# Kernel tuning notes

Measured on AMD Instinct MI355X. Metric: run time of the kernel, lower is better.

## Reference

```python
import jax, jax.numpy as jnp
import numpy as np

TOPK = 5

def setup_inputs() -> dict:
    key = jax.random.key(0)
    k1, k2, k3 = jax.random.split(key, 3)
    x = jax.random.normal(k1, (32, 256, 28, 28), jnp.float32)
    gamma = jnp.ones((256,), jnp.float32)
    beta = jnp.zeros((256,), jnp.float32)
    conv_w = jax.random.normal(k2, (256, 256), jnp.float32) * 0.02
    conv_b = jax.random.normal(k3, (256,), jnp.float32) * 0.02
    return {"x": x, "gamma": gamma, "beta": beta, "conv_w": conv_w, "conv_b": conv_b, "snip": 8}


def reference(x, gamma, beta, conv_w, conv_b, snip):
    BS, C, H, W = x.shape
    B = BS // snip
    THW = snip * H * W
    identity = x
    # [B_S,C,H,W] -> [B,C,THW] grouping snip frames per clip
    xs = x.reshape(B, snip, C, H, W).transpose(0, 2, 1, 3, 4).reshape(B, C, THW)
    # cosine correlation: x^T x / (|x_t| |x_s|)
    up = jnp.einsum('bct,bcs->bts', xs, xs)                    # [B,THW,THW]
    nrm = jnp.sqrt(jnp.sum(xs * xs, axis=1))                   # [B,THW]
    corr = up / (nrm[:, :, None] * nrm[:, None, :])
    # mask per-frame diagonal blocks with -1 (exclude same-frame matches)
    blk = jnp.arange(THW) // (H * W)
    diag_block = blk[:, None] == blk[None, :]                  # [THW,THW]
    corr = jnp.where(diag_block[None], jnp.float32(-1.0), corr)
    # torch.topk(corr, k, dim=1): top-k along rows for each column j.
    # corr is symmetric post-mask; implement via top_k on transposed last axis.
    _, idx = jax.lax.top_k(corr.transpose(0, 2, 1), TOPK)      # [B,THW,k]
    idx = idx.transpose(0, 2, 1)                               # [B,k,THW]
    # gather: out[b,i,c,j] = xs[b,c, idx[b,i,j]]  (slicecollect, vectorized)
    gathered = jnp.take_along_axis(xs[:, None], idx[:, :, None, :], axis=3)  # [B,k,C,THW]
    y = gathered.max(axis=1)                                   # [B,C,THW] ('max' mode)
    y = y.reshape(B, C, snip, H, W).transpose(0, 2, 1, 3, 4).reshape(BS, C, H, W)
    # BatchNorm2d (training-mode batch stats, eps=1e-5)
    mean = y.mean(axis=(0, 2, 3))
    var = y.var(axis=(0, 2, 3))
    y = (y - mean[None, :, None, None]) * jax.lax.rsqrt(var + 1e-5)[None, :, None, None]
    y = y * gamma[None, :, None, None] + beta[None, :, None, None]
    y = jax.nn.relu(y)
    # 1x1 conv
    y = jnp.einsum('bchw,oc->bohw', y, conv_w) + conv_b[None, :, None, None]
    return y + identity
```

## Files before the change

kernel.cpp:

```cpp
#include <hip/hip_runtime.h>
#include <cfloat>
#include <cmath>

#define B_    4
#define SNIP  8
#define CCH   256
#define HW    784
#define THW   6272
#define NROWS 25088
#define TOPK  5
#define NTILE 49
#define NPAIR 1225

typedef _Float16 f16;
typedef f16   half8 __attribute__((ext_vector_type(8)));
typedef f16   half4 __attribute__((ext_vector_type(4)));
typedef float f32x4 __attribute__((ext_vector_type(4)));

__device__ __forceinline__ void ins5(float key, int idx, float tv[TOPK], int ti[TOPK]) {
    const bool c4 = key > tv[4];
    const bool c3 = key > tv[3];
    const bool c2 = key > tv[2];
    const bool c1 = key > tv[1];
    const bool c0 = key > tv[0];
    tv[4] = c3 ? tv[3] : (c4 ? key : tv[4]);
    ti[4] = c3 ? ti[3] : (c4 ? idx : ti[4]);
    tv[3] = c2 ? tv[2] : (c3 ? key : tv[3]);
    ti[3] = c2 ? ti[2] : (c3 ? idx : ti[3]);
    tv[2] = c1 ? tv[1] : (c2 ? key : tv[2]);
    ti[2] = c1 ? ti[1] : (c2 ? idx : ti[2]);
    tv[1] = c0 ? tv[0] : (c1 ? key : tv[1]);
    ti[1] = c0 ? ti[0] : (c1 ? idx : ti[1]);
    tv[0] = c0 ? key  : tv[0];
    ti[0] = c0 ? idx  : ti[0];
}

__device__ __forceinline__ void async16(const void* g, void* l) {
    __builtin_amdgcn_global_load_lds(
        (const __attribute__((address_space(1))) void*)g,
        (__attribute__((address_space(3))) void*)l, 16, 0, 0);
}

__global__ __launch_bounds__(256)
void transpose_norm_split_kernel(const float* __restrict__ x, f16* __restrict__ Xs,
                                 float* __restrict__ nrm) {
    __shared__ float T[256][33];
    const int bs = blockIdx.x;
    const int p0 = blockIdx.y * 32;
    const int b = bs >> 3, f = bs & 7;
    const int tid = threadIdx.x;

    const int pl = tid & 31, ch = tid >> 5;
    const int p = p0 + pl;
    if (p < HW) {
#pragma unroll
        for (int cc = 0; cc < 32; ++cc) {
            const int c = cc * 8 + ch;
            T[c][pl] = x[((size_t)bs * CCH + c) * HW + p];
        }
    }
    __syncthreads();

    const int rloc = tid >> 3, k = tid & 7;
    const int gp = p0 + rloc;
    const size_t trow = (size_t)b * THW + (size_t)f * HW + gp;

    float s = 0.0f;
    if (gp < HW) {
#pragma unroll
        for (int j = 0; j < 32; ++j) {
            const float v = T[k * 32 + j][rloc];
            s += v * v;
        }
    }
    s += __shfl_xor(s, 1, 64);
    s += __shfl_xor(s, 2, 64);
    s += __shfl_xor(s, 4, 64);

    if (gp < HW) {
        const float sq = sqrtf(s);
        const float rs = 1.0f / sq;
        if (k == 0) nrm[trow] = sq;
#pragma unroll
        for (int q = 0; q < 4; ++q) {
            half8 hv, lv;
#pragma unroll
            for (int j = 0; j < 8; ++j) {
                const float v = T[k * 32 + q * 8 + j][rloc] * rs;
                const f16 h = (f16)v;
                hv[j] = h;
                lv[j] = (f16)(v - (float)h);
            }
            *(half8*)(Xs + trow * 512 + k * 32 + q * 8) = hv;
            *(half8*)(Xs + trow * 512 + 256 + k * 32 + q * 8) = lv;
        }
    }
}

__device__ __forceinline__ void block_merge_store(
    const float (*tv)[TOPK], const int (*ti)[TOPK], char* smem,
    int tid, int wid, int q, int wc, int lm,
    int rslot, size_t gcol0,
    float* __restrict__ pval, unsigned short* __restrict__ pidx) {
    float* Mv = (float*)smem;
    unsigned short* Mi = (unsigned short*)(smem + 21120);
    const int slot = (wid >> 1) * 4 + q;
    __syncthreads();
#pragma unroll
    for (int j = 0; j < 4; ++j) {
        const int c128 = wc + 16 * j + lm;
#pragma unroll
        for (int s = 0; s < TOPK; ++s) {
            Mv[(slot * TOPK + s) * 132 + c128] = tv[j][s];
            Mi[(slot * TOPK + s) * 132 + c128] = (unsigned short)ti[j][s];
        }
    }
    __syncthreads();
    if (tid < 128) {
        float bv5[TOPK]; int bi5[TOPK];
#pragma unroll
        for (int s = 0; s < TOPK; ++s) { bv5[s] = -FLT_MAX; bi5[s] = 0; }
        for (int s = 0; s < 40; ++s) ins5(Mv[s * 132 + tid], (int)Mi[s * 132 + tid], bv5, bi5);
#pragma unroll
        for (int s = 0; s < TOPK; ++s) {
            const size_t o = ((size_t)(rslot * TOPK + s)) * NROWS + gcol0 + tid;
            pval[o] = bv5[s];
            pidx[o] = (unsigned short)bi5[s];
        }
    }
}

__global__ __launch_bounds__(256, 3)
void gram_sym_kernel(const f16* __restrict__ Xs,
                     float* __restrict__ pval, unsigned short* __restrict__ pidx) {
    __shared__ __align__(16) char smem[33280];
    f16* As = (f16*)smem;
    f16* Bs = As + 8192;
    float* TT = (float*)smem;

    const int tid = threadIdx.x;
    const int lane = tid & 63, wid = tid >> 6;
    const int wr = (wid >> 1) * 64, wc = (wid & 1) * 64;
    const int lm = lane & 15, q = lane >> 4;
    const int lm7 = lm & 7;
    const int b = blockIdx.z;

    const int p = blockIdx.x;
    int cj = (int)((sqrtf(8.0f * (float)p + 1.0f) - 1.0f) * 0.5f);
    while ((cj + 1) * (cj + 2) / 2 <= p) ++cj;
    while (cj * (cj + 1) / 2 > p) --cj;
    const int ri = p - cj * (cj + 1) / 2;
    const int t0 = ri * 128, j0 = cj * 128;

    const size_t bbase = (size_t)b * THW;
    const f16* Xb = Xs + bbase * 512;

    const int srow = tid >> 3;
    const int skk = (((tid & 7) ^ (srow & 7)) * 8);

    int loj[4];
#pragma unroll
    for (int j = 0; j < 4; ++j) loj[j] = ((j0 + wc + 16 * j + lm) / HW) * HW;

    float tv[4][TOPK];
    int   ti[4][TOPK];
#pragma unroll
    for (int j = 0; j < 4; ++j)
#pragma unroll
        for (int s = 0; s < TOPK; ++s) { tv[j][s] = -FLT_MAX; ti[j][s] = 0; }

    const int segA[3] = {0, 256, 0};
    const int segB[3] = {0, 0, 256};

    f32x4 acc[4][4];
#pragma unroll
    for (int i = 0; i < 4; ++i)
#pragma unroll
        for (int j = 0; j < 4; ++j) acc[i][j] = (f32x4)0.0f;

    for (int cc = 0; cc < 12; ++cc) {
        const int seg = cc >> 2, k64 = (cc & 3) * 64;
        const int aoff = segA[seg] + k64 + skk;
        const int boff = segB[seg] + k64 + skk;
#pragma unroll
        for (int pp = 0; pp < 4; ++pp)
            async16(Xb + (size_t)(t0 + srow + 32 * pp) * 512 + aoff,
                    smem + wid * 1024 + pp * 4096);
#pragma unroll
        for (int pp = 0; pp < 4; ++pp)
            async16(Xb + (size_t)(j0 + srow + 32 * pp) * 512 + boff,
                    smem + 16384 + wid * 1024 + pp * 4096);
        __syncthreads();
#pragma unroll
        for (int ks = 0; ks < 2; ++ks) {
            const int ku = (((4 * ks + q) ^ lm7) * 8);
            half8 av[4], bv[4];
#pragma unroll
            for (int i = 0; i < 4; ++i)
                av[i] = *(const half8*)(As + (wr + 16 * i + lm) * 64 + ku);
#pragma unroll
            for (int j = 0; j < 4; ++j)
                bv[j] = *(const half8*)(Bs + (wc + 16 * j + lm) * 64 + ku);
#pragma unroll
            for (int i = 0; i < 4; ++i)
#pragma unroll
                for (int j = 0; j < 4; ++j)
                    acc[i][j] = __builtin_amdgcn_mfma_f32_16x16x32_f16(av[i], bv[j], acc[i][j], 0, 0, 0);
        }
        __syncthreads();
    }

#pragma unroll
    for (int i = 0; i < 4; ++i) {
        const int tb = t0 + wr + 16 * i + 4 * q;
#pragma unroll
        for (int reg = 0; reg < 4; ++reg) {
            const int t = tb + reg;
#pragma unroll
            for (int j = 0; j < 4; ++j) {
                const float key = ((unsigned)(t - loj[j]) < (unsigned)HW)
                                  ? -FLT_MAX : acc[i][j][reg];
                ins5(key, t, tv[j], ti[j]);
            }
        }
    }
    block_merge_store(tv, ti, smem, tid, wid, q, wc, lm,
                      ri, bbase + (size_t)j0, pval, pidx);

    if (ri != cj) {
        int lo2[4];
#pragma unroll
        for (int j = 0; j < 4; ++j) lo2[j] = ((t0 + wc + 16 * j + lm) / HW) * HW;
        float tv2[4][TOPK];
        int   ti2[4][TOPK];
#pragma unroll
        for (int j = 0; j < 4; ++j)
#pragma unroll
            for (int s = 0; s < TOPK; ++s) { tv2[j][s] = -FLT_MAX; ti2[j][s] = 0; }
        const int wrb = wid >> 1;
#pragma unroll
        for (int h = 0; h < 2; ++h) {
            __syncthreads();
            if ((wid & 1) == h) {
#pragma unroll
                for (int i = 0; i < 4; ++i)
#pragma unroll
                    for (int j = 0; j < 4; ++j)
#pragma unroll
                        for (int reg = 0; reg < 4; ++reg)
                            TT[(wr + 16 * i + 4 * q + reg) * 65 + 16 * j + lm] = acc[i][j][reg];
            }
            __syncthreads();
#pragma unroll
            for (int ii = 0; ii < 2; ++ii) {
                const int spb = wrb * 32 + 16 * ii + 4 * q;
                const int sg0 = j0 + 64 * h + spb;
#pragma unroll
                for (int reg = 0; reg < 4; ++reg) {
                    const int sg = sg0 + reg;
#pragma unroll
                    for (int j = 0; j < 4; ++j) {
                        const float raw = TT[(wc + 16 * j + lm) * 65 + spb + reg];
                        const float key = ((unsigned)(sg - lo2[j]) < (unsigned)HW)
                                          ? -FLT_MAX : raw;
                        ins5(key, sg, tv2[j], ti2[j]);
                    }
                }
            }
        }
        block_merge_store(tv2, ti2, smem, tid, wid, q, wc, lm,
                          cj, bbase + (size_t)t0, pval, pidx);
    }
}

__global__ __launch_bounds__(256)
void merge_topk_sym_kernel(const float* __restrict__ pval, const unsigned short* __restrict__ pidx,
                           int* __restrict__ idx5) {
    __shared__ float Lv[4][TOPK][64];
    __shared__ unsigned short Li[4][TOPK][64];
    const int tid = threadIdx.x;
    const int part = tid >> 6, cl = tid & 63;
    const int col = blockIdx.x * 64 + cl;

    float bv5[TOPK]; int bi5[TOPK];
#pragma unroll
    for (int s = 0; s < TOPK; ++s) { bv5[s] = -FLT_MAX; bi5[s] = 0; }

    const int r0 = part * 13;
    const int r1 = (r0 + 13 < NTILE) ? r0 + 13 : NTILE;
    for (int r = r0; r < r1; ++r) {
#pragma unroll
        for (int s = 0; s < TOPK; ++s) {
            const size_t o = ((size_t)(r * TOPK + s)) * NROWS + col;
            ins5(pval[o], (int)pidx[o], bv5, bi5);
        }
    }
#pragma unroll
    for (int s = 0; s < TOPK; ++s) { Lv[part][s][cl] = bv5[s]; Li[part][s][cl] = (unsigned short)bi5[s]; }
    __syncthreads();
    if (tid < 64) {
        float cv[TOPK]; int ci[TOPK];
#pragma unroll
        for (int s = 0; s < TOPK; ++s) { cv[s] = -FLT_MAX; ci[s] = 0; }
#pragma unroll
        for (int pp = 0; pp < 4; ++pp)
#pragma unroll
            for (int s = 0; s < TOPK; ++s) ins5(Lv[pp][s][tid], (int)Li[pp][s][tid], cv, ci);
        int* op = idx5 + (size_t)col * TOPK;
#pragma unroll
        for (int s = 0; s < TOPK; ++s) op[s] = ci[s];
    }
}

__global__ __launch_bounds__(256)
void gather_bn_kernel(const f16* __restrict__ Xs, const float* __restrict__ nrm,
                      const int* __restrict__ idx5,
                      f16* __restrict__ yf, float* __restrict__ partial) {
    __shared__ float ls[2][4][256];
    const int tid = threadIdx.x;
    const int wid = tid >> 6, lane = tid & 63;
    const int row0 = blockIdx.x * 32 + wid * 8;
    float s1x = 0, s1y = 0, s1z = 0, s1w = 0;
    float s2x = 0, s2y = 0, s2z = 0, s2w = 0;
    for (int rr = 0; rr < 8; ++rr) {
        const int row = row0 + rr;
        const int b = row / THW;
        const int* id = idx5 + (size_t)row * TOPK;
        const f16* base = Xs + (size_t)b * THW * 512;
        const float* nb = nrm + (size_t)b * THW;
        float4 m = make_float4(-FLT_MAX, -FLT_MAX, -FLT_MAX, -FLT_MAX);
#pragma unroll
        for (int i = 0; i < TOPK; ++i) {
            const int t = id[i];
            const float nv = nb[t];
            const f16* rp = base + (size_t)t * 512 + lane * 4;
            const half4 h = *(const half4*)rp;
            const half4 l = *(const half4*)(rp + 256);
            m.x = fmaxf(m.x, ((float)h.x + (float)l.x) * nv);
            m.y = fmaxf(m.y, ((float)h.y + (float)l.y) * nv);
            m.z = fmaxf(m.z, ((float)h.z + (float)l.z) * nv);
            m.w = fmaxf(m.w, ((float)h.w + (float)l.w) * nv);
        }
        half4 ym; ym.x = (f16)m.x; ym.y = (f16)m.y; ym.z = (f16)m.z; ym.w = (f16)m.w;
        *(half4*)(yf + (size_t)row * CCH + lane * 4) = ym;
        s1x += m.x; s1y += m.y; s1z += m.z; s1w += m.w;
        s2x += m.x * m.x; s2y += m.y * m.y; s2z += m.z * m.z; s2w += m.w * m.w;
    }
    *(float4*)&ls[0][wid][lane * 4] = make_float4(s1x, s1y, s1z, s1w);
    *(float4*)&ls[1][wid][lane * 4] = make_float4(s2x, s2y, s2z, s2w);
    __syncthreads();
    const float a  = ls[0][0][tid] + ls[0][1][tid] + ls[0][2][tid] + ls[0][3][tid];
    const float b2 = ls[1][0][tid] + ls[1][1][tid] + ls[1][2][tid] + ls[1][3][tid];
    partial[(size_t)blockIdx.x * 512 + tid] = a;
    partial[(size_t)blockIdx.x * 512 + 256 + tid] = b2;
}

__global__ __launch_bounds__(256)
void bn_final_kernel(const float* __restrict__ partial, const float* __restrict__ gamma,
                     const float* __restrict__ beta, float* __restrict__ ab) {
    const int c = blockIdx.x;
    const int tid = threadIdx.x;
    float s1 = 0, s2 = 0;
    for (int p = tid; p < 784; p += 256) {
        s1 += partial[(size_t)p * 512 + c];
        s2 += partial[(size_t)p * 512 + 256 + c];
    }
    __shared__ float r1[256], r2[256];
    r1[tid] = s1; r2[tid] = s2;
    __syncthreads();
    for (int off = 128; off > 0; off >>= 1) {
        if (tid < off) { r1[tid] += r1[tid + off]; r2[tid] += r2[tid + off]; }
        __syncthreads();
    }
    if (tid == 0) {
        const float inv_n = 1.0f / 25088.0f;
        const float mean = r1[0] * inv_n;
        const float var  = r2[0] * inv_n - mean * mean;
        const float a = gamma[c] / sqrtf(var + 1e-5f);
        ab[c] = a;
        ab[256 + c] = beta[c] - mean * a;
    }
}

__global__ __launch_bounds__(256, 2)
void conv_f16_kernel(const f16* __restrict__ yf, const float* __restrict__ w,
                     const float* __restrict__ ab, const float* __restrict__ cb,
                     const float* __restrict__ x, float* __restrict__ out) {
    __shared__ __align__(16) f16 smem[2 * 128 * 64];
    f16* As = smem;
    f16* Ws = smem + 8192;

    const int tid = threadIdx.x;
    const int lane = tid & 63, wid = tid >> 6;
    const int wr = (wid >> 1) * 64, wc = (wid & 1) * 64;
    const int lm = lane & 15, q = lane >> 4;
    const int lm7 = lm & 7;
    const int R0 = blockIdx.x * 128;
    const int o0 = blockIdx.y * 128;
    const int g8 = (tid & 7) * 8;
    const int sr = tid >> 3;

    f32x4 acc[4][4];
#pragma unroll
    for (int i = 0; i < 4; ++i)
#pragma unroll
        for (int j = 0; j < 4; ++j) acc[i][j] = (f32x4)0.0f;

    float cbv[4];
#pragma unroll
    for (int j = 0; j < 4; ++j) cbv[j] = cb[o0 + wc + 16 * j + lm];

    for (int kc = 0; kc < CCH; kc += 64) {
        const int cbase = kc + g8;
        const float4 sa0 = *(const float4*)(ab + cbase);
        const float4 sa1 = *(const float4*)(ab + cbase + 4);
        const float4 sb0 = *(const float4*)(ab + 256 + cbase);
        const float4 sb1 = *(const float4*)(ab + 256 + cbase + 4);
#pragma unroll
        for (int p = 0; p < 4; ++p) {
            const int r = sr + 32 * p;
            const half8 hv = *(const half8*)(yf + (size_t)(R0 + r) * CCH + cbase);
            half8 z;
            z[0] = (f16)fmaxf(fmaf((float)hv[0], sa0.x, sb0.x), 0.0f);
            z[1] = (f16)fmaxf(fmaf((float)hv[1], sa0.y, sb0.y), 0.0f);
            z[2] = (f16)fmaxf(fmaf((float)hv[2], sa0.z, sb0.z), 0.0f);
            z[3] = (f16)fmaxf(fmaf((float)hv[3], sa0.w, sb0.w), 0.0f);
            z[4] = (f16)fmaxf(fmaf((float)hv[4], sa1.x, sb1.x), 0.0f);
            z[5] = (f16)fmaxf(fmaf((float)hv[5], sa1.y, sb1.y), 0.0f);
            z[6] = (f16)fmaxf(fmaf((float)hv[6], sa1.z, sb1.z), 0.0f);
            z[7] = (f16)fmaxf(fmaf((float)hv[7], sa1.w, sb1.w), 0.0f);
            *(half8*)(As + r * 64 + (((tid & 7) ^ (r & 7)) * 8)) = z;
        }
#pragma unroll
        for (int p = 0; p < 4; ++p) {
            const int ol = sr + 32 * p;
            const float4 w0 = *(const float4*)(w + (size_t)(o0 + ol) * CCH + cbase);
            const float4 w1 = *(const float4*)(w + (size_t)(o0 + ol) * CCH + cbase + 4);
            half8 z;
            z[0] = (f16)w0.x; z[1] = (f16)w0.y; z[2] = (f16)w0.z; z[3] = (f16)w0.w;
            z[4] = (f16)w1.x; z[5] = (f16)w1.y; z[6] = (f16)w1.z; z[7] = (f16)w1.w;
            *(half8*)(Ws + ol * 64 + (((tid & 7) ^ (ol & 7)) * 8)) = z;
        }
        __syncthreads();
#pragma unroll
        for (int ks = 0; ks < 2; ++ks) {
            const int ku = (((4 * ks + q) ^ lm7) * 8);
            half8 av[4], bv[4];
#pragma unroll
            for (int i = 0; i < 4; ++i)
                av[i] = *(const half8*)(As + (wr + 16 * i + lm) * 64 + ku);
#pragma unroll
            for (int j = 0; j < 4; ++j)
                bv[j] = *(const half8*)(Ws + (wc + 16 * j + lm) * 64 + ku);
#pragma unroll
            for (int i = 0; i < 4; ++i)
#pragma unroll
                for (int j = 0; j < 4; ++j)
                    acc[i][j] = __builtin_amdgcn_mfma_f32_16x16x32_f16(av[i], bv[j], acc[i][j], 0, 0, 0);
        }
        __syncthreads();
    }
#pragma unroll
    for (int i = 0; i < 4; ++i) {
#pragma unroll
        for (int reg = 0; reg < 4; ++reg) {
            const int R = R0 + wr + 16 * i + 4 * q + reg;
            const int bs = R / HW;
            const int hw = R - bs * HW;
#pragma unroll
            for (int j = 0; j < 4; ++j) {
                const int o = o0 + wc + 16 * j + lm;
                const size_t oi = ((size_t)bs * CCH + o) * HW + hw;
                out[oi] = acc[i][j][reg] + cbv[j] + x[oi];
            }
        }
    }
}

extern "C" void kernel_launch(void* const* d_in, const int* in_sizes, int n_in,
                              void* d_out, int out_size, void* d_ws, size_t ws_size,
                              hipStream_t stream) {
    const float* x      = (const float*)d_in[0];
    const float* gamma  = (const float*)d_in[1];
    const float* beta   = (const float*)d_in[2];
    const float* conv_w = (const float*)d_in[3];
    const float* conv_b = (const float*)d_in[4];
    float* out = (float*)d_out;

    float* ws = (float*)d_ws;
    f16*   Xsp  = (f16*)ws;
    f16*   yf   = (f16*)(ws + 6422528);
    float* nrm  = ws + 9633792;
    float* part = ws + 9658880;
    float* ab   = ws + 10060288;
    int*   idx5 = (int*)(ws + 10060800);
    float* pvalS = ws + 10186240;
    unsigned short* pidxS = (unsigned short*)(ws + 16332800);

    transpose_norm_split_kernel<<<dim3(32, 25), 256, 0, stream>>>(x, Xsp, nrm);
    gram_sym_kernel<<<dim3(NPAIR, 1, B_), 256, 0, stream>>>(Xsp, pvalS, pidxS);
    merge_topk_sym_kernel<<<NROWS / 64, 256, 0, stream>>>(pvalS, pidxS, idx5);
    gather_bn_kernel<<<NROWS / 32, 256, 0, stream>>>(Xsp, nrm, idx5, yf, part);
    bn_final_kernel<<<256, 256, 0, stream>>>(part, gamma, beta, ab);
    conv_f16_kernel<<<dim3(NROWS / 128, 2), 256, 0, stream>>>(yf, conv_w, ab, conv_b, x, out);
}
```

Baseline: 418.8 us.

## Skip diagonal-block masking on off-diagonal tiles and swizzle transpose scratch for occupancy

Computes per tile whether its row and column frame ranges overlap, and uses a template-specialised epilogue that drops the per-element same-frame mask test when they do not. The padded 65-stride transpose scratch becomes a 64-stride rotated-column swizzle, so shared memory fits in 32 KB. Launch bounds go from 3 to 4 blocks per SM. The higher occupancy target may force register spills given the large accumulator and top-k state, and having two epilogue copies increases code size.

```diff
diff --git a/kernel.cpp b/kernel.cpp
--- a/kernel.cpp
+++ b/kernel.cpp
@@ -41,6 +41,49 @@
         (__attribute__((address_space(3))) void*)l, 16, 0, 0);
 }
 
+__device__ __forceinline__ int tta(int row, int col) {
+    return (row << 6) | ((col + row) & 63);
+}
+
+template<bool FM>
+__device__ __forceinline__ void epi_norm(const f32x4 (&acc)[4][4], int t0wrq, const int (&loj)[4],
+                                         float (&tv)[4][TOPK], int (&ti)[4][TOPK]) {
+#pragma unroll
+    for (int i = 0; i < 4; ++i) {
+#pragma unroll
+        for (int reg = 0; reg < 4; ++reg) {
+            const int t = t0wrq + 16 * i + reg;
+#pragma unroll
+            for (int j = 0; j < 4; ++j) {
+                float key = acc[i][j][reg];
+                if (FM) key = ((unsigned)(t - loj[j]) < (unsigned)HW) ? -FLT_MAX : key;
+                ins5(key, t, tv[j], ti[j]);
+            }
+        }
+    }
+}
+
+template<bool FM>
+__device__ __forceinline__ void epi_tr(const float* TT, int wrb, int q, int wc, int lm,
+                                       int j0h, const int (&lo2)[4],
+                                       float (&tv2)[4][TOPK], int (&ti2)[4][TOPK]) {
+#pragma unroll
+    for (int ii = 0; ii < 2; ++ii) {
+        const int spb = wrb * 32 + 16 * ii + 4 * q;
+        const int sg0 = j0h + spb;
+#pragma unroll
+        for (int reg = 0; reg < 4; ++reg) {
+            const int sg = sg0 + reg;
+#pragma unroll
+            for (int j = 0; j < 4; ++j) {
+                float key = TT[tta(wc + 16 * j + lm, spb + reg)];
+                if (FM) key = ((unsigned)(sg - lo2[j]) < (unsigned)HW) ? -FLT_MAX : key;
+                ins5(key, sg, tv2[j], ti2[j]);
+            }
+        }
+    }
+}
+
 __global__ __launch_bounds__(256)
 void transpose_norm_split_kernel(const float* __restrict__ x, f16* __restrict__ Xs,
                                  float* __restrict__ nrm) {
@@ -130,10 +173,10 @@
     }
 }
 
-__global__ __launch_bounds__(256, 3)
+__global__ __launch_bounds__(256, 4)
 void gram_sym_kernel(const f16* __restrict__ Xs,
                      float* __restrict__ pval, unsigned short* __restrict__ pidx) {
-    __shared__ __align__(16) char smem[33280];
+    __shared__ __align__(16) char smem[32768];
     f16* As = (f16*)smem;
     f16* Bs = As + 8192;
     float* TT = (float*)smem;
@@ -152,6 +195,10 @@
     const int ri = p - cj * (cj + 1) / 2;
     const int t0 = ri * 128, j0 = cj * 128;
 
+    const int ftl = t0 / HW, fth = (t0 + 127) / HW;
+    const int fjl = j0 / HW, fjh = (j0 + 127) / HW;
+    const bool fmask = (ftl <= fjh) && (fjl <= fth);
+
     const size_t bbase = (size_t)b * THW;
     const f16* Xb = Xs + bbase * 512;
 
@@ -210,20 +257,9 @@
         __syncthreads();
     }
 
-#pragma unroll
-    for (int i = 0; i < 4; ++i) {
-        const int tb = t0 + wr + 16 * i + 4 * q;
-#pragma unroll
-        for (int reg = 0; reg < 4; ++reg) {
-            const int t = tb + reg;
-#pragma unroll
-            for (int j = 0; j < 4; ++j) {
-                const float key = ((unsigned)(t - loj[j]) < (unsigned)HW)
-                                  ? -FLT_MAX : acc[i][j][reg];
-                ins5(key, t, tv[j], ti[j]);
-            }
-        }
-    }
+    const int t0wrq = t0 + wr + 4 * q;
+    if (fmask) epi_norm<true >(acc, t0wrq, loj, tv, ti);
+    else       epi_norm<false>(acc, t0wrq, loj, tv, ti);
     block_merge_store(tv, ti, smem, tid, wid, q, wc, lm,
                       ri, bbase + (size_t)j0, pval, pidx);
 
@@ -248,25 +284,11 @@
                     for (int j = 0; j < 4; ++j)
 #pragma unroll
                         for (int reg = 0; reg < 4; ++reg)
-                            TT[(wr + 16 * i + 4 * q + reg) * 65 + 16 * j + lm] = acc[i][j][reg];
+                            TT[tta(wr + 16 * i + 4 * q + reg, 16 * j + lm)] = acc[i][j][reg];
             }
             __syncthreads();
-#pragma unroll
-            for (int ii = 0; ii < 2; ++ii) {
-                const int spb = wrb * 32 + 16 * ii + 4 * q;
-                const int sg0 = j0 + 64 * h + spb;
-#pragma unroll
-                for (int reg = 0; reg < 4; ++reg) {
-                    const int sg = sg0 + reg;
-#pragma unroll
-                    for (int j = 0; j < 4; ++j) {
-                        const float raw = TT[(wc + 16 * j + lm) * 65 + spb + reg];
-                        const float key = ((unsigned)(sg - lo2[j]) < (unsigned)HW)
-                                          ? -FLT_MAX : raw;
-                        ins5(key, sg, tv2[j], ti2[j]);
-                    }
-                }
-            }
+            if (fmask) epi_tr<true >(TT, wrb, q, wc, lm, j0 + 64 * h, lo2, tv2, ti2);
+            else       epi_tr<false>(TT, wrb, q, wc, lm, j0 + 64 * h, lo2, tv2, ti2);
         }
         block_merge_store(tv2, ti2, smem, tid, wid, q, wc, lm,
                           cj, bbase + (size_t)t0, pval, pidx);
```

Result: slower. 491.0 us (+17.3%).

## Fuse top-k merge into gather-BN kernel and vectorize conv epilogue stores

Applied to the files above, without the earlier changes.

The separate merge_topk kernel is folded into the gather/BN-stats kernel. Each block now merges the per-tile top-5 candidates for its 32 rows in shared memory and uses the indices directly, which removes one launch and the idx5 global round trip. In the 1x1-conv epilogue, the four accumulator registers per lane are written with one float4 residual load and one float4 store instead of four scalar accesses. That relies on the four rows staying contiguous within one image and 16-byte aligned, which holds because 784 is divisible by 4.

```diff
diff --git a/kernel.cpp b/kernel.cpp
--- a/kernel.cpp
+++ b/kernel.cpp
@@ -274,64 +274,63 @@
 }
 
 __global__ __launch_bounds__(256)
-void merge_topk_sym_kernel(const float* __restrict__ pval, const unsigned short* __restrict__ pidx,
-                           int* __restrict__ idx5) {
-    __shared__ float Lv[4][TOPK][64];
-    __shared__ unsigned short Li[4][TOPK][64];
+void merge_gather_bn_kernel(const f16* __restrict__ Xs, const float* __restrict__ nrm,
+                            const float* __restrict__ pval, const unsigned short* __restrict__ pidx,
+                            f16* __restrict__ yf, float* __restrict__ partial) {
+    __shared__ float ls[2][4][256];
+    __shared__ float Pv[8][TOPK][32];
+    __shared__ unsigned short Pi[8][TOPK][32];
+    __shared__ int Fi[32][TOPK];
     const int tid = threadIdx.x;
-    const int part = tid >> 6, cl = tid & 63;
-    const int col = blockIdx.x * 64 + cl;
-
-    float bv5[TOPK]; int bi5[TOPK];
-#pragma unroll
-    for (int s = 0; s < TOPK; ++s) { bv5[s] = -FLT_MAX; bi5[s] = 0; }
-
-    const int r0 = part * 13;
-    const int r1 = (r0 + 13 < NTILE) ? r0 + 13 : NTILE;
-    for (int r = r0; r < r1; ++r) {
-#pragma unroll
-        for (int s = 0; s < TOPK; ++s) {
-            const size_t o = ((size_t)(r * TOPK + s)) * NROWS + col;
-            ins5(pval[o], (int)pidx[o], bv5, bi5);
-        }
-    }
-#pragma unroll
-    for (int s = 0; s < TOPK; ++s) { Lv[part][s][cl] = bv5[s]; Li[part][s][cl] = (unsigned short)bi5[s]; }
-    __syncthreads();
-    if (tid < 64) {
+    const int row0 = blockIdx.x * 32;
+
+    {
+        const int part = tid >> 5, cl = tid & 31;
+        const int col = row0 + cl;
+        const int r0 = part * 6;
+        const int r1 = (part == 7) ? NTILE : (r0 + 6);
+        float bv5[TOPK]; int bi5[TOPK];
+#pragma unroll
+        for (int s = 0; s < TOPK; ++s) { bv5[s] = -FLT_MAX; bi5[s] = 0; }
+        for (int r = r0; r < r1; ++r) {
+#pragma unroll
+            for (int s = 0; s < TOPK; ++s) {
+                const size_t o = ((size_t)(r * TOPK + s)) * NROWS + col;
+                ins5(pval[o], (int)pidx[o], bv5, bi5);
+            }
+        }
+#pragma unroll
+        for (int s = 0; s < TOPK; ++s) { Pv[part][s][cl] = bv5[s]; Pi[part][s][cl] = (unsigned short)bi5[s]; }
+    }
+    __syncthreads();
+
+    if (tid < 32) {
         float cv[TOPK]; int ci[TOPK];
 #pragma unroll
         for (int s = 0; s < TOPK; ++s) { cv[s] = -FLT_MAX; ci[s] = 0; }
 #pragma unroll
-        for (int pp = 0; pp < 4; ++pp)
-#pragma unroll
-            for (int s = 0; s < TOPK; ++s) ins5(Lv[pp][s][tid], (int)Li[pp][s][tid], cv, ci);
-        int* op = idx5 + (size_t)col * TOPK;
-#pragma unroll
-        for (int s = 0; s < TOPK; ++s) op[s] = ci[s];
-    }
-}
-
-__global__ __launch_bounds__(256)
-void gather_bn_kernel(const f16* __restrict__ Xs, const float* __restrict__ nrm,
-                      const int* __restrict__ idx5,
-                      f16* __restrict__ yf, float* __restrict__ partial) {
-    __shared__ float ls[2][4][256];
-    const int tid = threadIdx.x;
+        for (int pp = 0; pp < 8; ++pp)
+#pragma unroll
+            for (int s = 0; s < TOPK; ++s) ins5(Pv[pp][s][tid], (int)Pi[pp][s][tid], cv, ci);
+#pragma unroll
+        for (int s = 0; s < TOPK; ++s) Fi[tid][s] = ci[s];
+    }
+    __syncthreads();
+
     const int wid = tid >> 6, lane = tid & 63;
-    const int row0 = blockIdx.x * 32 + wid * 8;
+    const int lrow0 = wid * 8;
     float s1x = 0, s1y = 0, s1z = 0, s1w = 0;
     float s2x = 0, s2y = 0, s2z = 0, s2w = 0;
     for (int rr = 0; rr < 8; ++rr) {
-        const int row = row0 + rr;
+        const int lrow = lrow0 + rr;
+        const int row = row0 + lrow;
         const int b = row / THW;
-        const int* id = idx5 + (size_t)row * TOPK;
         const f16* base = Xs + (size_t)b * THW * 512;
         const float* nb = nrm + (size_t)b * THW;
         float4 m = make_float4(-FLT_MAX, -FLT_MAX, -FLT_MAX, -FLT_MAX);
 #pragma unroll
         for (int i = 0; i < TOPK; ++i) {
-            const int t = id[i];
+            const int t = Fi[lrow][i];
             const float nv = nb[t];
             const f16* rp = base + (size_t)t * 512 + lane * 4;
             const half4 h = *(const half4*)rp;
@@ -462,17 +461,20 @@
     }
 #pragma unroll
     for (int i = 0; i < 4; ++i) {
-#pragma unroll
-        for (int reg = 0; reg < 4; ++reg) {
-            const int R = R0 + wr + 16 * i + 4 * q + reg;
-            const int bs = R / HW;
-            const int hw = R - bs * HW;
-#pragma unroll
-            for (int j = 0; j < 4; ++j) {
-                const int o = o0 + wc + 16 * j + lm;
-                const size_t oi = ((size_t)bs * CCH + o) * HW + hw;
-                out[oi] = acc[i][j][reg] + cbv[j] + x[oi];
-            }
+        const int Rb = R0 + wr + 16 * i + 4 * q;
+        const int bs = Rb / HW;
+        const int hw = Rb - bs * HW;
+#pragma unroll
+        for (int j = 0; j < 4; ++j) {
+            const int o = o0 + wc + 16 * j + lm;
+            const size_t oi = ((size_t)bs * CCH + o) * HW + hw;
+            const float4 xv = *(const float4*)(x + oi);
+            float4 ov;
+            ov.x = acc[i][j][0] + cbv[j] + xv.x;
+            ov.y = acc[i][j][1] + cbv[j] + xv.y;
+            ov.z = acc[i][j][2] + cbv[j] + xv.z;
+            ov.w = acc[i][j][3] + cbv[j] + xv.w;
+            *(float4*)(out + oi) = ov;
         }
     }
 }
@@ -493,14 +495,12 @@
     float* nrm  = ws + 9633792;
     float* part = ws + 9658880;
     float* ab   = ws + 10060288;
-    int*   idx5 = (int*)(ws + 10060800);
     float* pvalS = ws + 10186240;
     unsigned short* pidxS = (unsigned short*)(ws + 16332800);
 
     transpose_norm_split_kernel<<<dim3(32, 25), 256, 0, stream>>>(x, Xsp, nrm);
     gram_sym_kernel<<<dim3(NPAIR, 1, B_), 256, 0, stream>>>(Xsp, pvalS, pidxS);
-    merge_topk_sym_kernel<<<NROWS / 64, 256, 0, stream>>>(pvalS, pidxS, idx5);
-    gather_bn_kernel<<<NROWS / 32, 256, 0, stream>>>(Xsp, nrm, idx5, yf, part);
+    merge_gather_bn_kernel<<<NROWS / 32, 256, 0, stream>>>(Xsp, nrm, pvalS, pidxS, yf, part);
     bn_final_kernel<<<256, 256, 0, stream>>>(part, gamma, beta, ab);
     conv_f16_kernel<<<dim3(NROWS / 128, 2), 256, 0, stream>>>(yf, conv_w, ab, conv_b, x, out);
 }
```

Result: faster. 402.1 us (-4.0%).
